# Kernel optimization log

Hardware: AMD Instinct MI355X
Metric: run time of the kernel (lower is better)

## Reference

```python
import jax, jax.numpy as jnp
import numpy as np

B, C, N, H = 4, 64, 1024, 8
D = C // H  # per-head depth = 8


def _split_heads(t, heads, depth):
    # t: [B, C, N] -> [B, H, N, D]  (matches view(B,H,D,N).permute(0,1,3,2))
    b, c, n = t.shape
    return t.reshape(b, heads, depth, n).transpose(0, 1, 3, 2)


def setup_inputs() -> dict:
    key = jax.random.key(0)
    kx, kq, kk, kv = jax.random.split(key, 4)
    x = jax.random.normal(kx, (B, C, N), dtype=jnp.float32)
    # 1x1 Conv1d with bias=False == pointwise linear: weight [out, in]
    scale = 1.0 / np.sqrt(C)
    Wq = jax.random.normal(kq, (C, C), dtype=jnp.float32) * scale
    Wk = jax.random.normal(kk, (C, C), dtype=jnp.float32) * scale
    Wv = jax.random.normal(kv, (C, C), dtype=jnp.float32) * scale
    return {"x": x, "Wq": Wq, "Wk": Wk, "Wv": Wv}


def reference(x, Wq, Wk, Wv):
    # QKV 1x1 conv projections: [B,C,N] -> [B,C,N]
    q = _split_heads(jnp.einsum('oc,bcn->bon', Wq, x), H, D)  # [B,H,N,D]
    k = _split_heads(jnp.einsum('oc,bcn->bon', Wk, x), H, D)  # [B,H,N,D]
    v = _split_heads(jnp.einsum('oc,bcn->bon', Wv, x), H, D)  # [B,H,N,D]

    # global_sub attention: per-pair elementwise subtraction scores
    # energy: [B,H,Nq,Nk,D]
    inv_sqrt_d = jnp.float32(1.0 / np.sqrt(D))
    energy = (q[:, :, :, None, :] - k[:, :, None, :, :]) * inv_sqrt_d
    attn = jax.nn.softmax(energy, axis=-2)  # softmax over keys, per channel
    # per-channel weighted sum of values over keys -> [B,H,N,D]
    out = jnp.einsum('bhnmd,bhmd->bhnd', attn, v)

    # variation returns [B,N,H,D]; forward then reshape(B,N,-1).permute(0,2,1)
    out = out.transpose(0, 2, 1, 3).reshape(x.shape[0], x.shape[2], -1)  # [B,N,C]
    return out.transpose(0, 2, 1)  # [B,C,N]
```

## Files before the change

### kernel.cpp

```cpp
#include <hip/hip_runtime.h>

#define BATCH 4
#define CH    64
#define NSEQ  1024
#define INV_SQRT_D 0.35355339059327373f


__global__ __launch_bounds__(1024)
void global_sub_attn_kernel(const float* __restrict__ x,
                            const float* __restrict__ Wk,
                            const float* __restrict__ Wv,
                            float* __restrict__ out)
{
    const int bc   = blockIdx.x;
    const int b    = bc >> 6;
    const int c    = bc & 63;
    const int n    = threadIdx.x;
    const int lane = n & 63;
    const int wave = n >> 6;

    __shared__ float wk_s[CH];
    __shared__ float wv_s[CH];
    __shared__ float red_a[16];
    __shared__ float red_b[16];

    if (n < CH)            wk_s[n]      = Wk[c * CH + n];
    else if (n < 2 * CH)   wv_s[n - CH] = Wv[c * CH + (n - CH)];
    __syncthreads();

    const float* xb = x + (size_t)b * CH * NSEQ + n;
    float kacc = 0.f, vacc = 0.f;
    #pragma unroll
    for (int cp = 0; cp < CH; ++cp) {
        const float xv = xb[cp * NSEQ];
        kacc = fmaf(wk_s[cp], xv, kacc);
        vacc = fmaf(wv_s[cp], xv, vacc);
    }

    const float e  = __expf(-kacc * INV_SQRT_D);
    float se  = e;
    float sev = e * vacc;

    #pragma unroll
    for (int off = 32; off > 0; off >>= 1) {
        se  += __shfl_xor(se,  off);
        sev += __shfl_xor(sev, off);
    }
    if (lane == 0) { red_a[wave] = se; red_b[wave] = sev; }
    __syncthreads();

    float tse = 0.f, tsev = 0.f;
    #pragma unroll
    for (int w = 0; w < 16; ++w) { tse += red_a[w]; tsev += red_b[w]; }

    out[(size_t)bc * NSEQ + n] = tsev / tse;
}

extern "C" void kernel_launch(void* const* d_in, const int* in_sizes, int n_in,
                              void* d_out, int out_size, void* d_ws, size_t ws_size,
                              hipStream_t stream) {
    const float* x  = (const float*)d_in[0];
    const float* Wk = (const float*)d_in[2];
    const float* Wv = (const float*)d_in[3];
    float* out = (float*)d_out;

    global_sub_attn_kernel<<<BATCH * CH, 1024, 0, stream>>>(x, Wk, Wv, out);
}
```

Baseline: 10.20 us.

## Split sequence reduction across four blocks with partial-sum workspace and broadcast kernel

Each (batch, channel) row's key reduction is split over four 256-thread blocks. Each block writes its partial exp-sum and exp-weighted value sum to workspace, and a second kernel combines the four partials and writes the output row with float4 stores. The aim is more, smaller blocks for better occupancy and wave scheduling on the GPU. In exchange it adds a second kernel launch and a round trip through global memory.

```diff
diff --git a/kernel.cpp b/kernel.cpp
--- a/kernel.cpp
+++ b/kernel.cpp
@@ -3,29 +3,33 @@
 #define BATCH 4
 #define CH    64
 #define NSEQ  1024
+#define NQUARTER 256
 #define INV_SQRT_D 0.35355339059327373f
 
 
-__global__ __launch_bounds__(1024)
-void global_sub_attn_kernel(const float* __restrict__ x,
-                            const float* __restrict__ Wk,
-                            const float* __restrict__ Wv,
-                            float* __restrict__ out)
+__global__ __launch_bounds__(256)
+void attn_partial_kernel(const float* __restrict__ x,
+                         const float* __restrict__ Wk,
+                         const float* __restrict__ Wv,
+                         float2* __restrict__ part)
 {
-    const int bc   = blockIdx.x;
+    const int blk  = blockIdx.x;
+    const int bc   = blk >> 2;
+    const int q    = blk & 3;
     const int b    = bc >> 6;
     const int c    = bc & 63;
-    const int n    = threadIdx.x;
-    const int lane = n & 63;
-    const int wave = n >> 6;
+    const int tid  = threadIdx.x;
+    const int lane = tid & 63;
+    const int wave = tid >> 6;
+    const int n    = q * NQUARTER + tid;
 
     __shared__ float wk_s[CH];
     __shared__ float wv_s[CH];
-    __shared__ float red_a[16];
-    __shared__ float red_b[16];
+    __shared__ float red_a[4];
+    __shared__ float red_b[4];
 
-    if (n < CH)            wk_s[n]      = Wk[c * CH + n];
-    else if (n < 2 * CH)   wv_s[n - CH] = Wv[c * CH + (n - CH)];
+    if (tid < CH)          wk_s[tid]      = Wk[c * CH + tid];
+    else if (tid < 2 * CH) wv_s[tid - CH] = Wv[c * CH + (tid - CH)];
     __syncthreads();
 
     const float* xb = x + (size_t)b * CH * NSEQ + n;
@@ -37,7 +41,7 @@
         vacc = fmaf(wv_s[cp], xv, vacc);
     }
 
-    const float e  = __expf(-kacc * INV_SQRT_D);
+    const float e = __expf(-kacc * INV_SQRT_D);
     float se  = e;
     float sev = e * vacc;
 
@@ -49,11 +53,31 @@
     if (lane == 0) { red_a[wave] = se; red_b[wave] = sev; }
     __syncthreads();
 
-    float tse = 0.f, tsev = 0.f;
-    #pragma unroll
-    for (int w = 0; w < 16; ++w) { tse += red_a[w]; tsev += red_b[w]; }
+    if (tid == 0) {
+        float2 p;
+        p.x = red_a[0] + red_a[1] + red_a[2] + red_a[3];
+        p.y = red_b[0] + red_b[1] + red_b[2] + red_b[3];
+        part[blk] = p;
+    }
+}
 
-    out[(size_t)bc * NSEQ + n] = tsev / tse;
+__global__ __launch_bounds__(256)
+void attn_broadcast_kernel(const float2* __restrict__ part,
+                           float* __restrict__ out)
+{
+    const int bc  = blockIdx.x;
+    const int tid = threadIdx.x;
+
+    const float2 p0 = part[bc * 4 + 0];
+    const float2 p1 = part[bc * 4 + 1];
+    const float2 p2 = part[bc * 4 + 2];
+    const float2 p3 = part[bc * 4 + 3];
+    const float tse  = (p0.x + p1.x) + (p2.x + p3.x);
+    const float tsev = (p0.y + p1.y) + (p2.y + p3.y);
+    const float o = tsev / tse;
+
+    float4 ov; ov.x = o; ov.y = o; ov.z = o; ov.w = o;
+    *reinterpret_cast<float4*>(out + (size_t)bc * NSEQ + tid * 4) = ov;
 }
 
 extern "C" void kernel_launch(void* const* d_in, const int* in_sizes, int n_in,
@@ -63,6 +87,8 @@
     const float* Wk = (const float*)d_in[2];
     const float* Wv = (const float*)d_in[3];
     float* out = (float*)d_out;
+    float2* part = (float2*)d_ws;
 
-    global_sub_attn_kernel<<<BATCH * CH, 1024, 0, stream>>>(x, Wk, Wv, out);
+    attn_partial_kernel<<<BATCH * CH * 4, 256, 0, stream>>>(x, Wk, Wv, part);
+    attn_broadcast_kernel<<<BATCH * CH, 256, 0, stream>>>(part, out);
 }
```

Result: slower. 11.82 us (+15.8%).

## Compute two output channels per block with float2 loads over sequence

Applied to the files above, without the earlier changes.

Each block now handles two output channels, splitting its 1024 threads into two groups of 512. Each thread covers two sequence positions using float2 loads of x and float4 shared-memory weight reads. This halves the grid and doubles the work per thread, aiming to cut instruction overhead and improve load width. x is no longer shared between the two channel groups within a block, so total global reads of x stay about the same while block count drops.

```diff
diff --git a/kernel.cpp b/kernel.cpp
--- a/kernel.cpp
+++ b/kernel.cpp
@@ -12,34 +12,54 @@
                             const float* __restrict__ Wv,
                             float* __restrict__ out)
 {
-    const int bc   = blockIdx.x;
-    const int b    = bc >> 6;
-    const int c    = bc & 63;
-    const int n    = threadIdx.x;
-    const int lane = n & 63;
-    const int wave = n >> 6;
+    const int blk   = blockIdx.x;
+    const int b     = blk >> 5;
+    const int cpair = blk & 31;
+    const int tid   = threadIdx.x;
+    const int g     = tid >> 9;
+    const int j     = tid & 511;
+    const int lane  = tid & 63;
+    const int wave  = tid >> 6;
 
-    __shared__ float wk_s[CH];
-    __shared__ float wv_s[CH];
+    __shared__ __align__(16) float wk_s[2][CH];
+    __shared__ __align__(16) float wv_s[2][CH];
     __shared__ float red_a[16];
     __shared__ float red_b[16];
 
-    if (n < CH)            wk_s[n]      = Wk[c * CH + n];
-    else if (n < 2 * CH)   wv_s[n - CH] = Wv[c * CH + (n - CH)];
+    if (tid < 256) {
+        const int gg = (tid >> 6) & 1;
+        const int cp = tid & 63;
+        const int cc = cpair * 2 + gg;
+        if (tid < 128) wk_s[gg][cp] = Wk[cc * CH + cp];
+        else           wv_s[gg][cp] = Wv[cc * CH + cp];
+    }
     __syncthreads();
 
-    const float* xb = x + (size_t)b * CH * NSEQ + n;
-    float kacc = 0.f, vacc = 0.f;
-    #pragma unroll
-    for (int cp = 0; cp < CH; ++cp) {
-        const float xv = xb[cp * NSEQ];
-        kacc = fmaf(wk_s[cp], xv, kacc);
-        vacc = fmaf(wv_s[cp], xv, vacc);
+    const float* xb = x + (size_t)b * CH * NSEQ + 2 * j;
+    float k0 = 0.f, k1 = 0.f, v0 = 0.f, v1 = 0.f;
+
+    #pragma unroll 4
+    for (int cp4 = 0; cp4 < CH; cp4 += 4) {
+        const float4 wk4 = *reinterpret_cast<const float4*>(&wk_s[g][cp4]);
+        const float4 wv4 = *reinterpret_cast<const float4*>(&wv_s[g][cp4]);
+        const float2 x0 = *reinterpret_cast<const float2*>(xb + (cp4 + 0) * NSEQ);
+        const float2 x1 = *reinterpret_cast<const float2*>(xb + (cp4 + 1) * NSEQ);
+        const float2 x2 = *reinterpret_cast<const float2*>(xb + (cp4 + 2) * NSEQ);
+        const float2 x3 = *reinterpret_cast<const float2*>(xb + (cp4 + 3) * NSEQ);
+        k0 = fmaf(wk4.x, x0.x, k0); k1 = fmaf(wk4.x, x0.y, k1);
+        v0 = fmaf(wv4.x, x0.x, v0); v1 = fmaf(wv4.x, x0.y, v1);
+        k0 = fmaf(wk4.y, x1.x, k0); k1 = fmaf(wk4.y, x1.y, k1);
+        v0 = fmaf(wv4.y, x1.x, v0); v1 = fmaf(wv4.y, x1.y, v1);
+        k0 = fmaf(wk4.z, x2.x, k0); k1 = fmaf(wk4.z, x2.y, k1);
+        v0 = fmaf(wv4.z, x2.x, v0); v1 = fmaf(wv4.z, x2.y, v1);
+        k0 = fmaf(wk4.w, x3.x, k0); k1 = fmaf(wk4.w, x3.y, k1);
+        v0 = fmaf(wv4.w, x3.x, v0); v1 = fmaf(wv4.w, x3.y, v1);
     }
 
-    const float e  = __expf(-kacc * INV_SQRT_D);
-    float se  = e;
-    float sev = e * vacc;
+    const float e0 = __expf(-k0 * INV_SQRT_D);
+    const float e1 = __expf(-k1 * INV_SQRT_D);
+    float se  = e0 + e1;
+    float sev = e0 * v0 + e1 * v1;
 
     #pragma unroll
     for (int off = 32; off > 0; off >>= 1) {
@@ -51,9 +71,12 @@
 
     float tse = 0.f, tsev = 0.f;
     #pragma unroll
-    for (int w = 0; w < 16; ++w) { tse += red_a[w]; tsev += red_b[w]; }
+    for (int w = 0; w < 8; ++w) { tse += red_a[g * 8 + w]; tsev += red_b[g * 8 + w]; }
+    const float o = tsev / tse;
 
-    out[(size_t)bc * NSEQ + n] = tsev / tse;
+    const int c = cpair * 2 + g;
+    float2 ov; ov.x = o; ov.y = o;
+    *reinterpret_cast<float2*>(out + ((size_t)b * CH + c) * NSEQ + 2 * j) = ov;
 }
 
 extern "C" void kernel_launch(void* const* d_in, const int* in_sizes, int n_in,
@@ -64,5 +87,5 @@
     const float* Wv = (const float*)d_in[3];
     float* out = (float*)d_out;
 
-    global_sub_attn_kernel<<<BATCH * CH, 1024, 0, stream>>>(x, Wk, Wv, out);
+    global_sub_attn_kernel<<<BATCH * (CH / 2), 1024, 0, stream>>>(x, Wk, Wv, out);
 }
```

Result: slower. 18.03 us (+76.8%).
